# Kernel optimization log

Measured on AMD Instinct MI355X. Metric: run time of the kernel, lower is better.

Reference implementation:

```python
import jax, jax.numpy as jnp
import numpy as np

N = 100000
E = 1600000
D_IN = 256
D_OUT = 128
ALPHA = 0.2  # LeakyReLU negative slope


def setup_inputs() -> dict:
    key = jax.random.key(0)
    k1, k2, k3, k4, k5 = jax.random.split(key, 5)
    x = jax.random.normal(k1, (N, D_IN), dtype=jnp.float32)
    # random edges + self-loops so every destination row has >=1 incoming edge
    src = jax.random.randint(k2, (E - N,), 0, N)
    dst = jax.random.randint(k3, (E - N,), 0, N)
    loops = jnp.arange(N)
    edge = jnp.stack([jnp.concatenate([src, loops]),
                      jnp.concatenate([dst, loops])]).astype(jnp.int64)  # [2, E]
    W = jax.random.normal(k4, (D_IN, D_OUT), dtype=jnp.float32) * 0.1
    a = jax.random.normal(k5, (1, 2 * D_OUT), dtype=jnp.float32) * 0.1
    return {"x": x, "edge": edge, "W": W, "a": a}


def reference(x, edge, W, a):
    n = x.shape[0]
    d_out = W.shape[1]
    h = x @ W  # [n, d_out]
    src, dst = edge[0], edge[1]
    # a @ concat(h[src], h[dst]) decomposes into two per-node projections
    f_src = h @ a[0, :d_out]   # [n]
    f_dst = h @ a[0, d_out:]   # [n]
    tmp = f_src[src] + f_dst[dst]                      # [E]
    lrelu = jnp.where(tmp > 0, tmp, ALPHA * tmp)
    edge_e = jnp.exp(-lrelu)                           # [E]
    # spmm(A, ones) -> rowsum; spmm(A, h) -> weighted aggregation (rows = src)
    e_rowsum = jax.ops.segment_sum(edge_e, src, num_segments=n)           # [n]
    hh = jax.ops.segment_sum(edge_e[:, None] * h[dst], src, num_segments=n)  # [n, d_out]
    hh = hh / e_rowsum[:, None]
    return jax.nn.elu(hh)  # end=False -> apply ELU
```

## Files before the change

### kernel.cpp

```cpp
#include <hip/hip_runtime.h>

#define D_IN 256
#define D_OUT 128
#define ALPHA 0.2f
#define RB 64
#define RBSH 6
#define NBMAX 1600
#define CH 8192
#define CAPG 1536
#define OVFCAP 32768
#define LKH 128

typedef __attribute__((ext_vector_type(8))) short bf16x8;
typedef __attribute__((ext_vector_type(4))) float f32x4;

__device__ inline unsigned short f2bf(float f) {
    unsigned int u = __float_as_uint(f);
    return (unsigned short)((u + 0x7FFFu + ((u >> 16) & 1u)) >> 16);
}
__device__ inline float bf2f(unsigned short u) {
    return __uint_as_float(((unsigned int)u) << 16);
}

__global__ __launch_bounds__(256) void k_wt(const float* __restrict__ W,
                                            unsigned short* __restrict__ WTb) {
    const int ncol = blockIdx.x;
    const int k = threadIdx.x;
    WTb[(size_t)ncol * 256 + k] = f2bf(W[(size_t)k * 128 + ncol]);
}

__global__ __launch_bounds__(256) void k_gemm(const float* __restrict__ x,
                                              const unsigned short* __restrict__ WTb,
                                              const float* __restrict__ a,
                                              unsigned short* __restrict__ hb,
                                              float* __restrict__ f_src,
                                              float* __restrict__ f_dst, int n) {
    __shared__ unsigned short sA[128 * LKH];
    __shared__ float sFp[128][2][2];
    const int t = threadIdx.x;
    const int l = t & 63;
    const int w = t >> 6;
    const int wr = w >> 1, wc = w & 1;
    const int row0 = blockIdx.x * 128;
    const int col0 = wc * 64;
    const int lr = l & 15;
    const int g = l >> 4;
    const int lk8 = g * 8;

    f32x4 acc[4][4] = {};
    const unsigned short* bp[4];
    #pragma unroll
    for (int ni = 0; ni < 4; ++ni)
        bp[ni] = WTb + (size_t)(col0 + ni * 16 + lr) * 256 + lk8;

    #pragma unroll
    for (int half = 0; half < 2; ++half) {
        {
            const int rr = t >> 4;
            const int cc = (t & 15) * 8;
            #pragma unroll
            for (int it = 0; it < 8; ++it) {
                int r = it * 16 + rr;
                int gr = row0 + r;
                float4 fa, fb;
                if (gr < n) {
                    const float* xp = &x[(size_t)gr * D_IN + half * LKH + cc];
                    fa = *(const float4*)xp;
                    fb = *(const float4*)(xp + 4);
                } else {
                    fa = make_float4(0.f, 0.f, 0.f, 0.f);
                    fb = fa;
                }
                bf16x8 v;
                v[0] = (short)f2bf(fa.x); v[1] = (short)f2bf(fa.y);
                v[2] = (short)f2bf(fa.z); v[3] = (short)f2bf(fa.w);
                v[4] = (short)f2bf(fb.x); v[5] = (short)f2bf(fb.y);
                v[6] = (short)f2bf(fb.z); v[7] = (short)f2bf(fb.w);
                int js = (cc >> 3) ^ ((r & 7) << 1);
                *(bf16x8*)&sA[r * LKH + js * 8] = v;
            }
        }
        __syncthreads();

        #pragma unroll
        for (int k0 = 0; k0 < LKH; k0 += 32) {
            bf16x8 af[4], bfr[4];
            #pragma unroll
            for (int mi = 0; mi < 4; ++mi) {
                int row_l = wr * 64 + mi * 16 + lr;
                int js = ((k0 >> 3) + g) ^ ((row_l & 7) << 1);
                af[mi] = *(const bf16x8*)&sA[row_l * LKH + js * 8];
            }
            #pragma unroll
            for (int ni = 0; ni < 4; ++ni)
                bfr[ni] = *(const bf16x8*)(bp[ni] + half * LKH + k0);
            #pragma unroll
            for (int mi = 0; mi < 4; ++mi)
                #pragma unroll
                for (int ni = 0; ni < 4; ++ni)
                    acc[mi][ni] = __builtin_amdgcn_mfma_f32_16x16x32_bf16(
                        af[mi], bfr[ni], acc[mi][ni], 0, 0, 0);
        }
        __syncthreads();
    }

    #pragma unroll
    for (int mi = 0; mi < 4; ++mi) {
        #pragma unroll
        for (int q = 0; q < 4; ++q) {
            int r = row0 + wr * 64 + mi * 16 + g * 4 + q;
            if (r < n) {
                #pragma unroll
                for (int ni = 0; ni < 4; ++ni)
                    hb[(size_t)r * D_OUT + col0 + ni * 16 + lr] =
                        f2bf(acc[mi][ni][q]);
            }
        }
    }

    float asv[4], adv[4];
    #pragma unroll
    for (int ni = 0; ni < 4; ++ni) {
        asv[ni] = a[col0 + ni * 16 + lr];
        adv[ni] = a[D_OUT + col0 + ni * 16 + lr];
    }
    #pragma unroll
    for (int mi = 0; mi < 4; ++mi) {
        #pragma unroll
        for (int q = 0; q < 4; ++q) {
            float fs = 0.f, fd = 0.f;
            #pragma unroll
            for (int ni = 0; ni < 4; ++ni) {
                float v = acc[mi][ni][q];
                fs = fmaf(v, asv[ni], fs);
                fd = fmaf(v, adv[ni], fd);
            }
            #pragma unroll
            for (int m = 1; m < 16; m <<= 1) {
                fs += __shfl_xor(fs, m);
                fd += __shfl_xor(fd, m);
            }
            if (lr == 0) {
                int rl = wr * 64 + mi * 16 + g * 4 + q;
                sFp[rl][wc][0] = fs;
                sFp[rl][wc][1] = fd;
            }
        }
    }
    __syncthreads();
    if (t < 128) {
        int r = row0 + t;
        if (r < n) {
            f_src[r] = sFp[t][0][0] + sFp[t][1][0];
            f_dst[r] = sFp[t][0][1] + sFp[t][1][1];
        }
    }
}

__global__ __launch_bounds__(256) void k_bfill(const int* __restrict__ src,
                                               const int* __restrict__ dst,
                                               int* __restrict__ gcnt,
                                               int2* __restrict__ ovf,
                                               int* __restrict__ gkeys, int E, int nb) {
    __shared__ int cnt[NBMAX];
    __shared__ int bas[NBMAX];
    const int t = threadIdx.x;
    const int e0 = blockIdx.x * CH;
    const int e1 = min(e0 + CH, E);
    for (int i = t; i < nb; i += 256) cnt[i] = 0;
    __syncthreads();
    for (int e = e0 + t; e < e1; e += 256) atomicAdd(&cnt[src[e] >> RBSH], 1);
    __syncthreads();
    for (int b = t; b < nb; b += 256) {
        int c = cnt[b];
        bas[b] = c ? atomicAdd(&gcnt[b], c) : 0;
        cnt[b] = 0;
    }
    __syncthreads();
    for (int e = e0 + t; e < e1; e += 256) {
        int s = src[e], d = dst[e];
        int b = s >> RBSH;
        int key = ((s & (RB - 1)) << 17) | d;
        int r = bas[b] + atomicAdd(&cnt[b], 1);
        if (r < CAPG) {
            gkeys[b * CAPG + r] = key;
        } else {
            int o = atomicAdd(&gcnt[nb], 1);
            if (o < OVFCAP) ovf[o] = make_int2(b, key);
        }
    }
}

__global__ __launch_bounds__(512, 8) void k_bagg(const unsigned short* __restrict__ hb,
                                                 const float* __restrict__ f_src,
                                                 const float* __restrict__ f_dst,
                                                 const int* __restrict__ gcnt,
                                                 const int2* __restrict__ ovf,
                                                 const int* __restrict__ gkeys,
                                                 float* __restrict__ out, int n, int nb) {
    __shared__ int2 sdw[CAPG];
    __shared__ int nbase[RB];
    __shared__ int ncnt[RB];
    __shared__ int ncur[RB];
    __shared__ float fsl[RB];
    __shared__ int sc[RB];
    const int t = threadIdx.x;
    const int b = blockIdx.x;
    const int s0 = b * RB;
    const int nn = min(RB, n - s0);
    const int beg = b * CAPG;
    const int stored = min(gcnt[b], CAPG);
    const int ovf_n = min(gcnt[nb], OVFCAP);

    for (int i = t; i < RB; i += 512) {
        ncnt[i] = 0;
        fsl[i] = (i < nn) ? f_src[s0 + i] : 0.f;
    }
    __syncthreads();

    for (int i = t; i < stored; i += 512)
        atomicAdd(&ncnt[gkeys[beg + i] >> 17], 1);
    __syncthreads();

    if (t < RB) sc[t] = ncnt[t];
    __syncthreads();
    for (int off = 1; off < RB; off <<= 1) {
        int v = 0;
        if (t < RB && t >= off) v = sc[t - off];
        __syncthreads();
        if (t < RB) sc[t] += v;
        __syncthreads();
    }
    if (t < RB) {
        nbase[t] = sc[t] - ncnt[t];
        ncur[t]  = sc[t] - ncnt[t];
    }
    __syncthreads();

    for (int i = t; i < stored; i += 512) {
        int k = gkeys[beg + i];
        int d = k & 0x1FFFF, ls = k >> 17;
        float tmp = fsl[ls] + f_dst[d];
        float w = __expf(-((tmp > 0.f) ? tmp : ALPHA * tmp));
        int pos = atomicAdd(&ncur[ls], 1);
        sdw[pos] = make_int2(d, __float_as_int(w));
    }
    __syncthreads();

    const int lane = t & 63, wid = t >> 6;
    const int cl = (lane & 31) * 4;
    const bool isB = lane >= 32;
    for (int ni = wid; ni < nn; ni += 8) {
        const int jb = nbase[ni];
        const int cn = ncnt[ni];
        const int halfA = (cn + 1) >> 1;
        const int halfB = cn - halfA;
        const int lim = isB ? halfB : halfA;
        const int jbh = jb + (isB ? halfA : 0);
        float a0 = 0.f, a1 = 0.f, a2 = 0.f, a3 = 0.f, rowsum = 0.f;
        #pragma unroll 4
        for (int it = 0; it < halfA; ++it) {
            bool valid = it < lim;
            int2 dw = sdw[valid ? (jbh + it) : jb];
            float w = valid ? __int_as_float(dw.y) : 0.f;
            ushort4 hv = *(const ushort4*)&hb[(size_t)dw.x * D_OUT + cl];
            rowsum += w;
            a0 = fmaf(w, bf2f(hv.x), a0);
            a1 = fmaf(w, bf2f(hv.y), a1);
            a2 = fmaf(w, bf2f(hv.z), a2);
            a3 = fmaf(w, bf2f(hv.w), a3);
        }
        if (ovf_n > 0) {
            for (int o = 0; o < ovf_n; ++o) {
                int2 ov = ovf[o];
                if (ov.x == b && (ov.y >> 17) == ni && !isB) {
                    int d = ov.y & 0x1FFFF;
                    float tmp = fsl[ni] + f_dst[d];
                    float w = __expf(-((tmp > 0.f) ? tmp : ALPHA * tmp));
                    ushort4 hv = *(const ushort4*)&hb[(size_t)d * D_OUT + cl];
                    rowsum += w;
                    a0 = fmaf(w, bf2f(hv.x), a0);
                    a1 = fmaf(w, bf2f(hv.y), a1);
                    a2 = fmaf(w, bf2f(hv.z), a2);
                    a3 = fmaf(w, bf2f(hv.w), a3);
                }
            }
        }
        rowsum += __shfl_xor(rowsum, 32);
        a0 += __shfl_xor(a0, 32);
        a1 += __shfl_xor(a1, 32);
        a2 += __shfl_xor(a2, 32);
        a3 += __shfl_xor(a3, 32);
        if (!isB) {
            float inv = 1.f / rowsum;
            a0 *= inv; a1 *= inv; a2 *= inv; a3 *= inv;
            a0 = (a0 > 0.f) ? a0 : (__expf(a0) - 1.f);
            a1 = (a1 > 0.f) ? a1 : (__expf(a1) - 1.f);
            a2 = (a2 > 0.f) ? a2 : (__expf(a2) - 1.f);
            a3 = (a3 > 0.f) ? a3 : (__expf(a3) - 1.f);
            *(float4*)&out[(size_t)(s0 + ni) * D_OUT + cl] =
                make_float4(a0, a1, a2, a3);
        }
    }
}

extern "C" void kernel_launch(void* const* d_in, const int* in_sizes, int n_in,
                              void* d_out, int out_size, void* d_ws, size_t ws_size,
                              hipStream_t stream) {
    const float* x    = (const float*)d_in[0];
    const int*   edge = (const int*)d_in[1];
    const float* W    = (const float*)d_in[2];
    const float* a    = (const float*)d_in[3];
    float* out = (float*)d_out;

    const int n = in_sizes[0] / D_IN;
    const int E = in_sizes[1] / 2;
    const int* src = edge;
    const int* dst = edge + E;
    const int nb = (n + RB - 1) / RB;

    char* p = (char*)d_ws;
    unsigned short* hb  = (unsigned short*)p; p += (size_t)n * D_OUT * sizeof(unsigned short);
    unsigned short* WTb = (unsigned short*)p; p += (size_t)D_OUT * D_IN * sizeof(unsigned short);
    float* f_src = (float*)p;  p += (size_t)n * sizeof(float);
    float* f_dst = (float*)p;  p += (size_t)n * sizeof(float);
    int*  gcnt   = (int*)p;    p += (size_t)(nb + 1) * sizeof(int);
    int2* ovf    = (int2*)p;   p += (size_t)OVFCAP * sizeof(int2);
    int*  gkeys  = (int*)p;    p += (size_t)nb * CAPG * sizeof(int);

    const int gemm_blocks = (n + 127) / 128;

    k_wt<<<D_OUT, 256, 0, stream>>>(W, WTb);
    k_gemm<<<gemm_blocks, 256, 0, stream>>>(x, WTb, a, hb, f_src, f_dst, n);

    hipMemsetAsync(gcnt, 0, (size_t)(nb + 1) * sizeof(int), stream);
    k_bfill<<<(E + CH - 1) / CH, 256, 0, stream>>>(src, dst, gcnt, ovf, gkeys, E, nb);
    k_bagg<<<nb, 512, 0, stream>>>(hb, f_src, f_dst, gcnt, ovf, gkeys, out, n, nb);
}
```

Measured before the change: 152.2 us.

## Split edges across four 16-lane groups with 16-byte bf16 gathers in aggregation

The aggregation kernel now gives each wavefront one node, split into four 16-lane groups. Each lane loads 8 bf16 values (16 bytes) per edge instead of 4, and the groups are reduced with two xor-shuffles. The block size drops from 512 to 256 threads, so each block handles its 64 nodes with 4 waves. The bucket-fill chunk size is also halved, giving twice as many fill blocks. The goal is wider memory transactions and more edges in flight per wave, at the cost of more shuffle reductions, more accumulator registers, and fewer waves per block to cover the serial edge loops.

```diff
diff --git a/kernel.cpp b/kernel.cpp
--- a/kernel.cpp
+++ b/kernel.cpp
@@ -6,7 +6,7 @@
 #define RB 64
 #define RBSH 6
 #define NBMAX 1600
-#define CH 8192
+#define CH 4096
 #define CAPG 1536
 #define OVFCAP 32768
 #define LKH 128
@@ -191,7 +191,7 @@
     }
 }
 
-__global__ __launch_bounds__(512, 8) void k_bagg(const unsigned short* __restrict__ hb,
+__global__ __launch_bounds__(256, 8) void k_bagg(const unsigned short* __restrict__ hb,
                                                  const float* __restrict__ f_src,
                                                  const float* __restrict__ f_dst,
                                                  const int* __restrict__ gcnt,
@@ -212,13 +212,13 @@
     const int stored = min(gcnt[b], CAPG);
     const int ovf_n = min(gcnt[nb], OVFCAP);
 
-    for (int i = t; i < RB; i += 512) {
+    for (int i = t; i < RB; i += 256) {
         ncnt[i] = 0;
         fsl[i] = (i < nn) ? f_src[s0 + i] : 0.f;
     }
     __syncthreads();
 
-    for (int i = t; i < stored; i += 512)
+    for (int i = t; i < stored; i += 256)
         atomicAdd(&ncnt[gkeys[beg + i] >> 17], 1);
     __syncthreads();
 
@@ -237,7 +237,7 @@
     }
     __syncthreads();
 
-    for (int i = t; i < stored; i += 512) {
+    for (int i = t; i < stored; i += 256) {
         int k = gkeys[beg + i];
         int d = k & 0x1FFFF, ls = k >> 17;
         float tmp = fsl[ls] + f_dst[d];
@@ -248,58 +248,63 @@
     __syncthreads();
 
     const int lane = t & 63, wid = t >> 6;
-    const int cl = (lane & 31) * 4;
-    const bool isB = lane >= 32;
-    for (int ni = wid; ni < nn; ni += 8) {
+    const int g = lane >> 4;
+    const int c0 = (lane & 15) * 8;
+    for (int ni = wid; ni < nn; ni += 4) {
         const int jb = nbase[ni];
         const int cn = ncnt[ni];
-        const int halfA = (cn + 1) >> 1;
-        const int halfB = cn - halfA;
-        const int lim = isB ? halfB : halfA;
-        const int jbh = jb + (isB ? halfA : 0);
-        float a0 = 0.f, a1 = 0.f, a2 = 0.f, a3 = 0.f, rowsum = 0.f;
+        float ac[8] = {};
+        float rowsum = 0.f;
+        const int iters = (cn + 3) >> 2;
         #pragma unroll 4
-        for (int it = 0; it < halfA; ++it) {
-            bool valid = it < lim;
-            int2 dw = sdw[valid ? (jbh + it) : jb];
+        for (int it = 0; it < iters; ++it) {
+            int idx = it * 4 + g;
+            bool valid = idx < cn;
+            int2 dw = sdw[valid ? (jb + idx) : jb];
             float w = valid ? __int_as_float(dw.y) : 0.f;
-            ushort4 hv = *(const ushort4*)&hb[(size_t)dw.x * D_OUT + cl];
+            bf16x8 hv = *(const bf16x8*)&hb[(size_t)dw.x * D_OUT + c0];
             rowsum += w;
-            a0 = fmaf(w, bf2f(hv.x), a0);
-            a1 = fmaf(w, bf2f(hv.y), a1);
-            a2 = fmaf(w, bf2f(hv.z), a2);
-            a3 = fmaf(w, bf2f(hv.w), a3);
+            #pragma unroll
+            for (int q = 0; q < 8; ++q)
+                ac[q] = fmaf(w, bf2f((unsigned short)hv[q]), ac[q]);
         }
         if (ovf_n > 0) {
             for (int o = 0; o < ovf_n; ++o) {
                 int2 ov = ovf[o];
-                if (ov.x == b && (ov.y >> 17) == ni && !isB) {
+                if (ov.x == b && (ov.y >> 17) == ni && g == 0) {
                     int d = ov.y & 0x1FFFF;
                     float tmp = fsl[ni] + f_dst[d];
                     float w = __expf(-((tmp > 0.f) ? tmp : ALPHA * tmp));
-                    ushort4 hv = *(const ushort4*)&hb[(size_t)d * D_OUT + cl];
+                    bf16x8 hv = *(const bf16x8*)&hb[(size_t)d * D_OUT + c0];
                     rowsum += w;
-                    a0 = fmaf(w, bf2f(hv.x), a0);
-                    a1 = fmaf(w, bf2f(hv.y), a1);
-                    a2 = fmaf(w, bf2f(hv.z), a2);
-                    a3 = fmaf(w, bf2f(hv.w), a3);
+                    #pragma unroll
+                    for (int q = 0; q < 8; ++q)
+                        ac[q] = fmaf(w, bf2f((unsigned short)hv[q]), ac[q]);
                 }
             }
         }
+        rowsum += __shfl_xor(rowsum, 16);
         rowsum += __shfl_xor(rowsum, 32);
-        a0 += __shfl_xor(a0, 32);
-        a1 += __shfl_xor(a1, 32);
-        a2 += __shfl_xor(a2, 32);
-        a3 += __shfl_xor(a3, 32);
-        if (!isB) {
+        #pragma unroll
+        for (int q = 0; q < 8; ++q) {
+            ac[q] += __shfl_xor(ac[q], 16);
+            ac[q] += __shfl_xor(ac[q], 32);
+        }
+        if (lane < 16) {
             float inv = 1.f / rowsum;
-            a0 *= inv; a1 *= inv; a2 *= inv; a3 *= inv;
-            a0 = (a0 > 0.f) ? a0 : (__expf(a0) - 1.f);
-            a1 = (a1 > 0.f) ? a1 : (__expf(a1) - 1.f);
-            a2 = (a2 > 0.f) ? a2 : (__expf(a2) - 1.f);
-            a3 = (a3 > 0.f) ? a3 : (__expf(a3) - 1.f);
-            *(float4*)&out[(size_t)(s0 + ni) * D_OUT + cl] =
-                make_float4(a0, a1, a2, a3);
+            float4 o0, o1;
+            float v;
+            v = ac[0] * inv; o0.x = (v > 0.f) ? v : (__expf(v) - 1.f);
+            v = ac[1] * inv; o0.y = (v > 0.f) ? v : (__expf(v) - 1.f);
+            v = ac[2] * inv; o0.z = (v > 0.f) ? v : (__expf(v) - 1.f);
+            v = ac[3] * inv; o0.w = (v > 0.f) ? v : (__expf(v) - 1.f);
+            v = ac[4] * inv; o1.x = (v > 0.f) ? v : (__expf(v) - 1.f);
+            v = ac[5] * inv; o1.y = (v > 0.f) ? v : (__expf(v) - 1.f);
+            v = ac[6] * inv; o1.z = (v > 0.f) ? v : (__expf(v) - 1.f);
+            v = ac[7] * inv; o1.w = (v > 0.f) ? v : (__expf(v) - 1.f);
+            float* op = &out[(size_t)(s0 + ni) * D_OUT + c0];
+            *(float4*)op = o0;
+            *(float4*)(op + 4) = o1;
         }
     }
 }
@@ -335,5 +340,5 @@
 
     hipMemsetAsync(gcnt, 0, (size_t)(nb + 1) * sizeof(int), stream);
     k_bfill<<<(E + CH - 1) / CH, 256, 0, stream>>>(src, dst, gcnt, ovf, gkeys, E, nb);
-    k_bagg<<<nb, 512, 0, stream>>>(hb, f_src, f_dst, gcnt, ovf, gkeys, out, n, nb);
-}
+    k_bagg<<<nb, 256, 0, stream>>>(hb, f_src, f_dst, gcnt, ovf, gkeys, out, n, nb);
+}
```

New measurement: 155.3 us. 2.1% more time.
